# Performance work log

Hardware: AMD Instinct MI355X
Metric: run time of the kernel (lower is better)

Reference implementation:

```python
import jax, jax.numpy as jnp
import numpy as np

N_EMB, D_LAT, D_HID, D_MID, D_IN = 1024, 64, 256, 128, 9
BETA = 0.25  # commitment_cost
N = 262144


def _kaiming(k, shape):
    # kaiming_normal_ with nonlinearity='relu': std = sqrt(2 / fan_in)
    fan_in = shape[1]
    return jax.random.normal(k, shape, jnp.float32) * jnp.sqrt(jnp.float32(2.0 / fan_in))


def setup_inputs() -> dict:
    key = jax.random.key(0)
    ks = jax.random.split(key, 8)
    return {
        "x": jax.random.normal(ks[0], (N, D_IN), jnp.float32),
        # Encoder: Linear(9->256) ReLU Linear(256->128) ReLU Linear(128->64)
        "enc_w1": _kaiming(ks[1], (D_HID, D_IN)),  "enc_b1": jnp.zeros((D_HID,), jnp.float32),
        "enc_w2": _kaiming(ks[2], (D_MID, D_HID)), "enc_b2": jnp.zeros((D_MID,), jnp.float32),
        "enc_w3": _kaiming(ks[3], (D_LAT, D_MID)), "enc_b3": jnp.zeros((D_LAT,), jnp.float32),
        # Decoder: Linear(64->128) ReLU Linear(128->256) ReLU Linear(256->9)
        "dec_w1": _kaiming(ks[4], (D_MID, D_LAT)), "dec_b1": jnp.zeros((D_MID,), jnp.float32),
        "dec_w2": _kaiming(ks[5], (D_HID, D_MID)), "dec_b2": jnp.zeros((D_HID,), jnp.float32),
        "dec_w3": _kaiming(ks[6], (D_IN, D_HID)),  "dec_b3": jnp.zeros((D_IN,), jnp.float32),
        # Codebook: Embedding(1024, 64), uniform(-1, 1)
        "codebook": jax.random.uniform(ks[7], (N_EMB, D_LAT), jnp.float32, -1.0, 1.0),
    }


def _mlp3(h, w1, b1, w2, b2, w3, b3):
    h = jax.nn.relu(h @ w1.T + b1)
    h = jax.nn.relu(h @ w2.T + b2)
    return h @ w3.T + b3


def reference(x, enc_w1, enc_b1, enc_w2, enc_b2, enc_w3, enc_b3,
              dec_w1, dec_b1, dec_w2, dec_b2, dec_w3, dec_b3, codebook):
    z_e = _mlp3(x, enc_w1, enc_b1, enc_w2, enc_b2, enc_w3, enc_b3)  # [N, 64]
    # squared euclidean distances to codebook: [N, N_EMB]
    d = (jnp.sum(z_e * z_e, axis=1, keepdims=True)
         - 2.0 * (z_e @ codebook.T)
         + jnp.sum(codebook * codebook, axis=1))
    idx = jnp.argmin(d, axis=1)                 # [N] int
    quantized = codebook[idx]                   # gather == onehot @ codebook
    e_latent = jnp.mean((jax.lax.stop_gradient(quantized) - z_e) ** 2)
    q_latent = jnp.mean((quantized - jax.lax.stop_gradient(z_e)) ** 2)
    vq_loss = q_latent + BETA * e_latent
    # straight-through estimator
    z_q = z_e + jax.lax.stop_gradient(quantized - z_e)
    # perplexity from codebook usage histogram (== mean of one-hot encodings)
    counts = jnp.zeros((N_EMB,), jnp.float32).at[idx].add(1.0)
    avg_probs = counts / jnp.float32(z_e.shape[0])
    perplexity = jnp.exp(-jnp.sum(avg_probs * jnp.log(avg_probs + 1e-10)))
    x_recon = _mlp3(z_q, dec_w1, dec_b1, dec_w2, dec_b2, dec_w3, dec_b3)
    return (x_recon, vq_loss, perplexity)
```

## Files before the change

kernel.cpp:

```cpp
#include <hip/hip_runtime.h>
#include <math.h>


namespace {

constexpr int kN = 262144;

typedef _Float16 half8 __attribute__((ext_vector_type(8)));
typedef float floatx4 __attribute__((ext_vector_type(4)));

#define MFMA16(a, b, c) __builtin_amdgcn_mfma_f32_16x16x32_f16((a), (b), (c), 0, 0, 0)

constexpr size_t W1M_O = 0;
constexpr size_t W1R_O = 16384;
constexpr size_t E2M_O = 32768;
constexpr size_t E2R_O = 98304;
constexpr size_t E3M_O = 163840;
constexpr size_t E3R_O = 180224;
constexpr size_t CBM_O = 196608;
constexpr size_t CBR_O = 327680;
constexpr size_t D1P_O = 458752;
constexpr size_t D2P_O = 475136;
constexpr size_t D3P_O = 540672;
constexpr size_t CN_O  = 548864;
constexpr size_t IDX_O = 589824;
constexpr size_t ESP_O = IDX_O + 1048576;
constexpr size_t HP_O  = ESP_O + 32768;

__device__ __forceinline__ void split2(float v, _Float16& hi, _Float16& lo) {
  hi = (_Float16)v;
  lo = (_Float16)(v - (float)hi);
}

__global__ void prep_kernel(
    const float* __restrict__ ew1, const float* __restrict__ ew2,
    const float* __restrict__ ew3, const float* __restrict__ cb,
    const float* __restrict__ dw1, const float* __restrict__ dw2,
    const float* __restrict__ dw3, char* __restrict__ wsb) {
  _Float16* w1m = (_Float16*)(wsb + W1M_O);
  _Float16* w1r = (_Float16*)(wsb + W1R_O);
  _Float16* e2m = (_Float16*)(wsb + E2M_O);
  _Float16* e2r = (_Float16*)(wsb + E2R_O);
  _Float16* e3m = (_Float16*)(wsb + E3M_O);
  _Float16* e3r = (_Float16*)(wsb + E3R_O);
  _Float16* cbm = (_Float16*)(wsb + CBM_O);
  _Float16* cbr = (_Float16*)(wsb + CBR_O);
  _Float16* d1p = (_Float16*)(wsb + D1P_O);
  _Float16* d2p = (_Float16*)(wsb + D2P_O);
  _Float16* d3p = (_Float16*)(wsb + D3P_O);
  float* cn = (float*)(wsb + CN_O);

  const int gid = blockIdx.x * 256 + threadIdx.x;
  const int stride = gridDim.x * 256;
  for (int e = gid; e < 256 * 32; e += stride) {
    int n = e >> 5, k = e & 31;
    float v = (k < 9) ? ew1[n * 9 + k] : 0.f;
    split2(v, w1m[e], w1r[e]);
  }
  for (int e = gid; e < 128 * 256; e += stride) split2(ew2[e], e2m[e], e2r[e]);
  for (int e = gid; e < 64 * 128; e += stride) split2(ew3[e], e3m[e], e3r[e]);
  for (int e = gid; e < 1024 * 64; e += stride) split2(cb[e], cbm[e], cbr[e]);
  for (int e = gid; e < 128 * 64; e += stride) d1p[e] = (_Float16)dw1[e];
  for (int e = gid; e < 256 * 128; e += stride) d2p[e] = (_Float16)dw2[e];
  for (int e = gid; e < 16 * 256; e += stride) {
    int n = e >> 8, k = e & 255;
    d3p[e] = (n < 9) ? (_Float16)dw3[n * 256 + k] : (_Float16)0.f;
  }
  for (int i = gid; i < 1024; i += stride) {
    float s = 0.f;
    const float* c = cb + (size_t)i * 64;
#pragma unroll 8
    for (int k = 0; k < 64; ++k) s = fmaf(c[k], c[k], s);
    cn[i] = s;
  }
}

__global__ __launch_bounds__(256, 3) void vqvae_mega(
    const float* __restrict__ x,
    const float* __restrict__ eb1, const float* __restrict__ eb2,
    const float* __restrict__ eb3, const float* __restrict__ db1,
    const float* __restrict__ db2, const float* __restrict__ db3,
    const float* __restrict__ cb, const char* __restrict__ wsb,
    float* __restrict__ out, int* __restrict__ idx_g, float* __restrict__ esp_g) {
  __shared__ _Float16 LP[20480];

  const int t = threadIdx.x;
  const int lane = t & 63;
  const int w = t >> 6;
  const int m = lane & 15;
  const int q = lane >> 4;
  const int R0 = blockIdx.x * 128;
  const int wr0 = 32 * w;
  _Float16* WPS = LP + 10240 + w * 2560;
  const float* cn_g = (const float*)(wsb + CN_O);

  half8 axm[2] = {{}, {}}, axr[2] = {{}, {}};
#pragma unroll
  for (int rt = 0; rt < 2; ++rt) {
    const int grow = R0 + wr0 + 16 * rt + m;
    if (q == 0) {
#pragma unroll
      for (int j = 0; j < 8; ++j) {
        const float v = x[(size_t)grow * 9 + j];
        const _Float16 hi = (_Float16)v;
        axm[rt][j] = hi;
        axr[rt][j] = (_Float16)(v - (float)hi);
      }
    } else if (q == 1) {
      const float v = x[(size_t)grow * 9 + 8];
      const _Float16 hi = (_Float16)v;
      axm[rt][0] = hi;
      axr[rt][0] = (_Float16)(v - (float)hi);
    }
  }

  floatx4 acc2[8][2];
#pragma unroll
  for (int nt = 0; nt < 8; ++nt)
#pragma unroll
    for (int rt = 0; rt < 2; ++rt) acc2[nt][rt] = (floatx4){0.f, 0.f, 0.f, 0.f};

  for (int kc = 0; kc < 8; ++kc) {
    __syncthreads();
    {
      const int p = t >> 7, n = t & 127;
      const char* src = wsb + (p ? E2R_O : E2M_O) + (size_t)n * 512 + kc * 64;
      _Float16* dst = LP + (p ? 5120 : 0) + n * 40;
#pragma unroll
      for (int j = 0; j < 4; ++j)
        *(half8*)(dst + j * 8) = *(const half8*)(src + j * 16);
    }
#pragma unroll
    for (int ntl = 0; ntl < 2; ++ntl) {
      const int f = kc * 32 + ntl * 16 + m;
      const half8 bm = *(const half8*)(wsb + W1M_O + (size_t)f * 64 + q * 16);
      const half8 br = *(const half8*)(wsb + W1R_O + (size_t)f * 64 + q * 16);
      const float bias = eb1[f];
#pragma unroll
      for (int rt = 0; rt < 2; ++rt) {
        floatx4 a = (floatx4){0.f, 0.f, 0.f, 0.f};
        a = MFMA16(axr[rt], bm, a);
        a = MFMA16(axm[rt], br, a);
        a = MFMA16(axm[rt], bm, a);
#pragma unroll
        for (int reg = 0; reg < 4; ++reg) {
          const float v = fmaxf(a[reg] + bias, 0.f);
          const int row = 16 * rt + 4 * q + reg;
          const _Float16 hi = (_Float16)v;
          WPS[row * 40 + ntl * 16 + m] = hi;
          WPS[1280 + row * 40 + ntl * 16 + m] = (_Float16)(v - (float)hi);
        }
      }
    }
    __syncthreads();
    half8 am[2], ar[2];
#pragma unroll
    for (int rt = 0; rt < 2; ++rt) {
      am[rt] = *(const half8*)(WPS + (16 * rt + m) * 40 + q * 8);
      ar[rt] = *(const half8*)(WPS + 1280 + (16 * rt + m) * 40 + q * 8);
    }
#pragma unroll
    for (int nt = 0; nt < 8; ++nt) {
      const half8 bm = *(const half8*)(LP + (nt * 16 + m) * 40 + q * 8);
      const half8 br = *(const half8*)(LP + 5120 + (nt * 16 + m) * 40 + q * 8);
#pragma unroll
      for (int rt = 0; rt < 2; ++rt) {
        acc2[nt][rt] = MFMA16(ar[rt], bm, acc2[nt][rt]);
        acc2[nt][rt] = MFMA16(am[rt], br, acc2[nt][rt]);
        acc2[nt][rt] = MFMA16(am[rt], bm, acc2[nt][rt]);
      }
    }
  }

  floatx4 acc3[4][2];
#pragma unroll
  for (int nt = 0; nt < 4; ++nt)
#pragma unroll
    for (int rt = 0; rt < 2; ++rt) acc3[nt][rt] = (floatx4){0.f, 0.f, 0.f, 0.f};

  for (int ks = 0; ks < 4; ++ks) {
#pragma unroll
    for (int h = 0; h < 2; ++h) {
      const int nt = 2 * ks + h;
      const float bias = eb2[nt * 16 + m];
#pragma unroll
      for (int rt = 0; rt < 2; ++rt) {
#pragma unroll
        for (int reg = 0; reg < 4; ++reg) {
          const float v = fmaxf(acc2[nt][rt][reg] + bias, 0.f);
          const int row = 16 * rt + 4 * q + reg;
          const _Float16 hi = (_Float16)v;
          WPS[row * 40 + h * 16 + m] = hi;
          WPS[1280 + row * 40 + h * 16 + m] = (_Float16)(v - (float)hi);
        }
      }
    }
    half8 am[2], ar[2];
#pragma unroll
    for (int rt = 0; rt < 2; ++rt) {
      am[rt] = *(const half8*)(WPS + (16 * rt + m) * 40 + q * 8);
      ar[rt] = *(const half8*)(WPS + 1280 + (16 * rt + m) * 40 + q * 8);
    }
#pragma unroll
    for (int nt = 0; nt < 4; ++nt) {
      const half8 bm = *(const half8*)(wsb + E3M_O + (size_t)(nt * 16 + m) * 256 + ks * 64 + q * 16);
      const half8 br = *(const half8*)(wsb + E3R_O + (size_t)(nt * 16 + m) * 256 + ks * 64 + q * 16);
#pragma unroll
      for (int rt = 0; rt < 2; ++rt) {
        acc3[nt][rt] = MFMA16(ar[rt], bm, acc3[nt][rt]);
        acc3[nt][rt] = MFMA16(am[rt], br, acc3[nt][rt]);
        acc3[nt][rt] = MFMA16(am[rt], bm, acc3[nt][rt]);
      }
    }
  }

  half8 zfm[2][2], zfr[2][2];
#pragma unroll
  for (int rt = 0; rt < 2; ++rt) {
#pragma unroll
    for (int nt = 0; nt < 4; ++nt) {
      const float bias = eb3[nt * 16 + m];
#pragma unroll
      for (int reg = 0; reg < 4; ++reg) {
        const float v = acc3[nt][rt][reg] + bias;
        const int row = 4 * q + reg;
        const _Float16 hi = (_Float16)v;
        WPS[row * 72 + nt * 16 + m] = hi;
        WPS[1152 + row * 72 + nt * 16 + m] = (_Float16)(v - (float)hi);
      }
    }
#pragma unroll
    for (int ks2 = 0; ks2 < 2; ++ks2) {
      zfm[rt][ks2] = *(const half8*)(WPS + m * 72 + ks2 * 32 + q * 8);
      zfr[rt][ks2] = *(const half8*)(WPS + 1152 + m * 72 + ks2 * 32 + q * 8);
    }
  }

  float bestd[2][4];
  int besti[2][4];
#pragma unroll
  for (int rt = 0; rt < 2; ++rt)
#pragma unroll
    for (int reg = 0; reg < 4; ++reg) { bestd[rt][reg] = 3.4e38f; besti[rt][reg] = 0; }

  for (int cc = 0; cc < 16; ++cc) {
    __syncthreads();
    {
      const int p = t >> 7, e = t & 127;
      const int n = e >> 1, hh = e & 1;
      const char* src = wsb + (p ? CBR_O : CBM_O) + (size_t)(cc * 64 + n) * 128 + hh * 64;
      _Float16* dst = LP + (p ? 4608 : 0) + n * 72 + hh * 32;
#pragma unroll
      for (int j = 0; j < 4; ++j)
        *(half8*)(dst + j * 8) = *(const half8*)(src + j * 16);
    }
    __syncthreads();
    floatx4 accd[4][2];
#pragma unroll
    for (int nt = 0; nt < 4; ++nt)
#pragma unroll
      for (int rt = 0; rt < 2; ++rt) accd[nt][rt] = (floatx4){0.f, 0.f, 0.f, 0.f};
#pragma unroll
    for (int nt = 0; nt < 4; ++nt) {
#pragma unroll
      for (int ks2 = 0; ks2 < 2; ++ks2) {
        const half8 bm = *(const half8*)(LP + (nt * 16 + m) * 72 + ks2 * 32 + q * 8);
        const half8 br = *(const half8*)(LP + 4608 + (nt * 16 + m) * 72 + ks2 * 32 + q * 8);
#pragma unroll
        for (int rt = 0; rt < 2; ++rt) {
          accd[nt][rt] = MFMA16(zfr[rt][ks2], bm, accd[nt][rt]);
          accd[nt][rt] = MFMA16(zfm[rt][ks2], br, accd[nt][rt]);
          accd[nt][rt] = MFMA16(zfm[rt][ks2], bm, accd[nt][rt]);
        }
      }
    }
#pragma unroll
    for (int nt = 0; nt < 4; ++nt) {
      const int code = cc * 64 + nt * 16 + m;
      const float cnv = cn_g[code];
#pragma unroll
      for (int rt = 0; rt < 2; ++rt) {
#pragma unroll
        for (int reg = 0; reg < 4; ++reg) {
          const float d = cnv - 2.f * accd[nt][rt][reg];
          if (d < bestd[rt][reg]) { bestd[rt][reg] = d; besti[rt][reg] = code; }
        }
      }
    }
  }
#pragma unroll
  for (int rt = 0; rt < 2; ++rt) {
#pragma unroll
    for (int reg = 0; reg < 4; ++reg) {
#pragma unroll
      for (int off = 1; off < 16; off <<= 1) {
        const float od = __shfl_xor(bestd[rt][reg], off, 16);
        const int oi = __shfl_xor(besti[rt][reg], off, 16);
        if (od < bestd[rt][reg] || (od == bestd[rt][reg] && oi < besti[rt][reg])) {
          bestd[rt][reg] = od; besti[rt][reg] = oi;
        }
      }
    }
  }
  if (m == 0) {
#pragma unroll
    for (int rt = 0; rt < 2; ++rt)
#pragma unroll
      for (int reg = 0; reg < 4; ++reg) {
        const int row = wr0 + 16 * rt + 4 * q + reg;
        idx_g[R0 + row] = besti[rt][reg];
      }
  }

  const int sl = ((m >> 2) << 4) | m;
  half8 zq[2][2];
  float es = 0.f;
#pragma unroll
  for (int rt = 0; rt < 2; ++rt) {
    const int b0 = __shfl(besti[rt][0], sl);
    const int b1 = __shfl(besti[rt][1], sl);
    const int b2 = __shfl(besti[rt][2], sl);
    const int b3 = __shfl(besti[rt][3], sl);
    const int r2 = m & 3;
    const int bi = (r2 == 0) ? b0 : (r2 == 1) ? b1 : (r2 == 2) ? b2 : b3;
#pragma unroll
    for (int ks2 = 0; ks2 < 2; ++ks2) {
      const float* cp = cb + (size_t)bi * 64 + ks2 * 32 + q * 8;
      const float4 c0 = *(const float4*)cp;
      const float4 c1 = *(const float4*)(cp + 4);
      float cv[8] = {c0.x, c0.y, c0.z, c0.w, c1.x, c1.y, c1.z, c1.w};
#pragma unroll
      for (int j = 0; j < 8; ++j) {
        const float z = (float)zfm[rt][ks2][j] + (float)zfr[rt][ks2][j];
        const float d = cv[j] - z;
        es = fmaf(d, d, es);
        zq[rt][ks2][j] = (_Float16)(z + d);
      }
    }
  }
#pragma unroll
  for (int off = 1; off < 64; off <<= 1) es += __shfl_xor(es, off, 64);
  if (lane == 0) esp_g[blockIdx.x * 4 + w] = es;

  floatx4 accH[8][2];
#pragma unroll
  for (int nt = 0; nt < 8; ++nt)
#pragma unroll
    for (int rt = 0; rt < 2; ++rt) accH[nt][rt] = (floatx4){0.f, 0.f, 0.f, 0.f};
#pragma unroll
  for (int nt = 0; nt < 8; ++nt) {
#pragma unroll
    for (int ks2 = 0; ks2 < 2; ++ks2) {
      const half8 b = *(const half8*)(wsb + D1P_O + (size_t)(nt * 16 + m) * 128 + ks2 * 64 + q * 16);
#pragma unroll
      for (int rt = 0; rt < 2; ++rt) accH[nt][rt] = MFMA16(zq[rt][ks2], b, accH[nt][rt]);
    }
  }
  half8 h3f[2][4];
  for (int ks = 0; ks < 4; ++ks) {
#pragma unroll
    for (int h = 0; h < 2; ++h) {
      const int nt = 2 * ks + h;
      const float bias = db1[nt * 16 + m];
#pragma unroll
      for (int rt = 0; rt < 2; ++rt)
#pragma unroll
        for (int reg = 0; reg < 4; ++reg) {
          const float v = fmaxf(accH[nt][rt][reg] + bias, 0.f);
          WPS[(16 * rt + 4 * q + reg) * 40 + h * 16 + m] = (_Float16)v;
        }
    }
#pragma unroll
    for (int rt = 0; rt < 2; ++rt)
      h3f[rt][ks] = *(const half8*)(WPS + (16 * rt + m) * 40 + q * 8);
  }

  floatx4 accO[2] = {(floatx4){0.f, 0.f, 0.f, 0.f}, (floatx4){0.f, 0.f, 0.f, 0.f}};
  for (int jc = 0; jc < 4; ++jc) {
    __syncthreads();
    {
      const int n = t >> 2, jj = t & 3;
      const char* src = wsb + D2P_O + (size_t)(jc * 64 + n) * 256 + jj * 64;
      _Float16* dst = LP + n * 136 + jj * 32;
#pragma unroll
      for (int j = 0; j < 4; ++j)
        *(half8*)(dst + j * 8) = *(const half8*)(src + j * 16);
    }
    __syncthreads();
    floatx4 accD2[4][2];
#pragma unroll
    for (int nt = 0; nt < 4; ++nt)
#pragma unroll
      for (int rt = 0; rt < 2; ++rt) accD2[nt][rt] = (floatx4){0.f, 0.f, 0.f, 0.f};
#pragma unroll
    for (int nt = 0; nt < 4; ++nt) {
#pragma unroll
      for (int ks = 0; ks < 4; ++ks) {
        const half8 b = *(const half8*)(LP + (nt * 16 + m) * 136 + ks * 32 + q * 8);
#pragma unroll
        for (int rt = 0; rt < 2; ++rt) accD2[nt][rt] = MFMA16(h3f[rt][ks], b, accD2[nt][rt]);
      }
    }
    half8 b3[2];
#pragma unroll
    for (int ks2 = 0; ks2 < 2; ++ks2)
      b3[ks2] = *(const half8*)(wsb + D3P_O + (size_t)m * 512 + jc * 128 + ks2 * 64 + q * 16);
#pragma unroll
    for (int rt = 0; rt < 2; ++rt) {
#pragma unroll
      for (int nt = 0; nt < 4; ++nt) {
        const float bias = db2[jc * 64 + nt * 16 + m];
#pragma unroll
        for (int reg = 0; reg < 4; ++reg) {
          const float v = fmaxf(accD2[nt][rt][reg] + bias, 0.f);
          WPS[(4 * q + reg) * 72 + nt * 16 + m] = (_Float16)v;
        }
      }
#pragma unroll
      for (int ks2 = 0; ks2 < 2; ++ks2) {
        const half8 am = *(const half8*)(WPS + m * 72 + ks2 * 32 + q * 8);
        accO[rt] = MFMA16(am, b3[ks2], accO[rt]);
      }
    }
  }
  if (m < 9) {
    const float bias = db3[m];
#pragma unroll
    for (int rt = 0; rt < 2; ++rt)
#pragma unroll
      for (int reg = 0; reg < 4; ++reg) {
        const size_t r = (size_t)(R0 + wr0 + 16 * rt + 4 * q + reg);
        out[r * 9 + m] = accO[rt][reg] + bias;
      }
  }
}

__global__ __launch_bounds__(256) void hist_kernel(
    const int* __restrict__ idx_g, int* __restrict__ hp) {
  __shared__ int lh[1024];
  const int t = threadIdx.x;
#pragma unroll
  for (int i = 0; i < 4; ++i) lh[t * 4 + i] = 0;
  __syncthreads();
  for (int i = t; i < 4096; i += 256)
    atomicAdd(&lh[idx_g[blockIdx.x * 4096 + i]], 1);
  __syncthreads();
  int* part = hp + blockIdx.x * 1024;
#pragma unroll
  for (int i = 0; i < 4; ++i) part[t * 4 + i] = lh[t * 4 + i];
}

__global__ __launch_bounds__(1024) void finalize_kernel(
    const int* __restrict__ hp, const float* __restrict__ esp,
    float* __restrict__ out2) {
  __shared__ double red[1024];
  __shared__ float rede[1024];
  const int t = threadIdx.x;
  int h = 0;
#pragma unroll 8
  for (int p = 0; p < 64; ++p) h += hp[p * 1024 + t];
  const float pr = (float)h * (1.0f / (float)kN);
  red[t] = (double)(pr * logf(pr + 1e-10f));
  float es = 0.f;
#pragma unroll
  for (int i = 0; i < 8; ++i) es += esp[i * 1024 + t];
  rede[t] = es;
  __syncthreads();
  for (int s = 512; s > 0; s >>= 1) {
    if (t < s) { red[t] += red[t + s]; rede[t] += rede[t + s]; }
    __syncthreads();
  }
  if (t == 0) {
    out2[0] = 1.25f * (rede[0] * (1.0f / ((float)kN * 64.0f)));
    out2[1] = expf((float)(-red[0]));
  }
}

}

extern "C" void kernel_launch(void* const* d_in, const int* in_sizes, int n_in,
                              void* d_out, int out_size, void* d_ws, size_t ws_size,
                              hipStream_t stream) {
  const float* x   = (const float*)d_in[0];
  const float* ew1 = (const float*)d_in[1];
  const float* eb1 = (const float*)d_in[2];
  const float* ew2 = (const float*)d_in[3];
  const float* eb2 = (const float*)d_in[4];
  const float* ew3 = (const float*)d_in[5];
  const float* eb3 = (const float*)d_in[6];
  const float* dw1 = (const float*)d_in[7];
  const float* db1 = (const float*)d_in[8];
  const float* dw2 = (const float*)d_in[9];
  const float* db2 = (const float*)d_in[10];
  const float* dw3 = (const float*)d_in[11];
  const float* db3 = (const float*)d_in[12];
  const float* cb  = (const float*)d_in[13];
  float* out = (float*)d_out;
  char* wsb = (char*)d_ws;

  int* idx_g = (int*)(wsb + IDX_O);
  float* esp = (float*)(wsb + ESP_O);
  int* hp = (int*)(wsb + HP_O);

  prep_kernel<<<128, 256, 0, stream>>>(ew1, ew2, ew3, cb, dw1, dw2, dw3, wsb);
  vqvae_mega<<<kN / 128, 256, 0, stream>>>(x, eb1, eb2, eb3, db1, db2, db3, cb,
                                           wsb, out, idx_g, esp);
  hist_kernel<<<64, 256, 0, stream>>>(idx_g, hp);
  finalize_kernel<<<1, 1024, 0, stream>>>(hp, esp, out + (size_t)kN * 9);
}
```

Baseline: 332.7 us.

## Load MFMA weight operands directly from global memory instead of staging in LDS

Drops the cooperative LDS staging of the encoder layer-2, codebook and decoder layer-2 weight tiles. Each wave now reads its B fragments straight from global memory (L1/L2-resident), which removes all the block-wide __syncthreads. Only per-wave scratch stays in shared memory, so LDS use halves, and waitcnt fences replace the barriers for intra-wave transposes. In exchange every wave issues redundant global loads of the same weights, adding L1/L2 traffic and latency that the MFMA loops may not hide.

```diff
diff --git a/kernel.cpp b/kernel.cpp
--- a/kernel.cpp
+++ b/kernel.cpp
@@ -10,6 +10,7 @@
 typedef float floatx4 __attribute__((ext_vector_type(4)));
 
 #define MFMA16(a, b, c) __builtin_amdgcn_mfma_f32_16x16x32_f16((a), (b), (c), 0, 0, 0)
+#define LDS_FENCE() asm volatile("s_waitcnt lgkmcnt(0)" ::: "memory")
 
 constexpr size_t W1M_O = 0;
 constexpr size_t W1R_O = 16384;
@@ -82,7 +83,7 @@
     const float* __restrict__ db2, const float* __restrict__ db3,
     const float* __restrict__ cb, const char* __restrict__ wsb,
     float* __restrict__ out, int* __restrict__ idx_g, float* __restrict__ esp_g) {
-  __shared__ _Float16 LP[20480];
+  __shared__ _Float16 LP[10240];
 
   const int t = threadIdx.x;
   const int lane = t & 63;
@@ -91,7 +92,7 @@
   const int q = lane >> 4;
   const int R0 = blockIdx.x * 128;
   const int wr0 = 32 * w;
-  _Float16* WPS = LP + 10240 + w * 2560;
+  _Float16* WPS = LP + w * 2560;
   const float* cn_g = (const float*)(wsb + CN_O);
 
   half8 axm[2] = {{}, {}}, axr[2] = {{}, {}};
@@ -121,15 +122,6 @@
     for (int rt = 0; rt < 2; ++rt) acc2[nt][rt] = (floatx4){0.f, 0.f, 0.f, 0.f};
 
   for (int kc = 0; kc < 8; ++kc) {
-    __syncthreads();
-    {
-      const int p = t >> 7, n = t & 127;
-      const char* src = wsb + (p ? E2R_O : E2M_O) + (size_t)n * 512 + kc * 64;
-      _Float16* dst = LP + (p ? 5120 : 0) + n * 40;
-#pragma unroll
-      for (int j = 0; j < 4; ++j)
-        *(half8*)(dst + j * 8) = *(const half8*)(src + j * 16);
-    }
 #pragma unroll
     for (int ntl = 0; ntl < 2; ++ntl) {
       const int f = kc * 32 + ntl * 16 + m;
@@ -152,7 +144,7 @@
         }
       }
     }
-    __syncthreads();
+    LDS_FENCE();
     half8 am[2], ar[2];
 #pragma unroll
     for (int rt = 0; rt < 2; ++rt) {
@@ -161,8 +153,8 @@
     }
 #pragma unroll
     for (int nt = 0; nt < 8; ++nt) {
-      const half8 bm = *(const half8*)(LP + (nt * 16 + m) * 40 + q * 8);
-      const half8 br = *(const half8*)(LP + 5120 + (nt * 16 + m) * 40 + q * 8);
+      const half8 bm = *(const half8*)(wsb + E2M_O + (size_t)(nt * 16 + m) * 512 + kc * 64 + q * 16);
+      const half8 br = *(const half8*)(wsb + E2R_O + (size_t)(nt * 16 + m) * 512 + kc * 64 + q * 16);
 #pragma unroll
       for (int rt = 0; rt < 2; ++rt) {
         acc2[nt][rt] = MFMA16(ar[rt], bm, acc2[nt][rt]);
@@ -195,6 +187,7 @@
         }
       }
     }
+    LDS_FENCE();
     half8 am[2], ar[2];
 #pragma unroll
     for (int rt = 0; rt < 2; ++rt) {
@@ -229,6 +222,7 @@
         WPS[1152 + row * 72 + nt * 16 + m] = (_Float16)(v - (float)hi);
       }
     }
+    LDS_FENCE();
 #pragma unroll
     for (int ks2 = 0; ks2 < 2; ++ks2) {
       zfm[rt][ks2] = *(const half8*)(WPS + m * 72 + ks2 * 32 + q * 8);
@@ -244,17 +238,6 @@
     for (int reg = 0; reg < 4; ++reg) { bestd[rt][reg] = 3.4e38f; besti[rt][reg] = 0; }
 
   for (int cc = 0; cc < 16; ++cc) {
-    __syncthreads();
-    {
-      const int p = t >> 7, e = t & 127;
-      const int n = e >> 1, hh = e & 1;
-      const char* src = wsb + (p ? CBR_O : CBM_O) + (size_t)(cc * 64 + n) * 128 + hh * 64;
-      _Float16* dst = LP + (p ? 4608 : 0) + n * 72 + hh * 32;
-#pragma unroll
-      for (int j = 0; j < 4; ++j)
-        *(half8*)(dst + j * 8) = *(const half8*)(src + j * 16);
-    }
-    __syncthreads();
     floatx4 accd[4][2];
 #pragma unroll
     for (int nt = 0; nt < 4; ++nt)
@@ -264,8 +247,8 @@
     for (int nt = 0; nt < 4; ++nt) {
 #pragma unroll
       for (int ks2 = 0; ks2 < 2; ++ks2) {
-        const half8 bm = *(const half8*)(LP + (nt * 16 + m) * 72 + ks2 * 32 + q * 8);
-        const half8 br = *(const half8*)(LP + 4608 + (nt * 16 + m) * 72 + ks2 * 32 + q * 8);
+        const half8 bm = *(const half8*)(wsb + CBM_O + (size_t)(cc * 64 + nt * 16 + m) * 128 + ks2 * 64 + q * 16);
+        const half8 br = *(const half8*)(wsb + CBR_O + (size_t)(cc * 64 + nt * 16 + m) * 128 + ks2 * 64 + q * 16);
 #pragma unroll
         for (int rt = 0; rt < 2; ++rt) {
           accd[nt][rt] = MFMA16(zfr[rt][ks2], bm, accd[nt][rt]);
@@ -370,6 +353,7 @@
           WPS[(16 * rt + 4 * q + reg) * 40 + h * 16 + m] = (_Float16)v;
         }
     }
+    LDS_FENCE();
 #pragma unroll
     for (int rt = 0; rt < 2; ++rt)
       h3f[rt][ks] = *(const half8*)(WPS + (16 * rt + m) * 40 + q * 8);
@@ -377,16 +361,6 @@
 
   floatx4 accO[2] = {(floatx4){0.f, 0.f, 0.f, 0.f}, (floatx4){0.f, 0.f, 0.f, 0.f}};
   for (int jc = 0; jc < 4; ++jc) {
-    __syncthreads();
-    {
-      const int n = t >> 2, jj = t & 3;
-      const char* src = wsb + D2P_O + (size_t)(jc * 64 + n) * 256 + jj * 64;
-      _Float16* dst = LP + n * 136 + jj * 32;
-#pragma unroll
-      for (int j = 0; j < 4; ++j)
-        *(half8*)(dst + j * 8) = *(const half8*)(src + j * 16);
-    }
-    __syncthreads();
     floatx4 accD2[4][2];
 #pragma unroll
     for (int nt = 0; nt < 4; ++nt)
@@ -396,7 +370,7 @@
     for (int nt = 0; nt < 4; ++nt) {
 #pragma unroll
       for (int ks = 0; ks < 4; ++ks) {
-        const half8 b = *(const half8*)(LP + (nt * 16 + m) * 136 + ks * 32 + q * 8);
+        const half8 b = *(const half8*)(wsb + D2P_O + (size_t)(jc * 64 + nt * 16 + m) * 256 + ks * 64 + q * 16);
 #pragma unroll
         for (int rt = 0; rt < 2; ++rt) accD2[nt][rt] = MFMA16(h3f[rt][ks], b, accD2[nt][rt]);
       }
@@ -416,6 +390,7 @@
           WPS[(4 * q + reg) * 72 + nt * 16 + m] = (_Float16)v;
         }
       }
+      LDS_FENCE();
 #pragma unroll
       for (int ks2 = 0; ks2 < 2; ++ks2) {
         const half8 am = *(const half8*)(WPS + m * 72 + ks2 * 32 + q * 8);
```

Result: slower. 633.2 us (+90.3%).
